# Kernel optimization log

Hardware: AMD Instinct MI355X
Metric: run time of the kernel (lower is better)

## Reference

```python
import jax, jax.numpy as jnp
import numpy as np
from jax import lax

KS = 3
PAD = 1


def setup_inputs() -> dict:
    key = jax.random.key(0)
    k1, k2, k3 = jax.random.split(key, 3)
    b, c, h, w = 8, 64, 128, 128
    out_c = 64
    x = jax.random.normal(k1, (b, c, h, w), dtype=jnp.float32)
    # small offset weights keep predicted offsets in a sane range
    w_off = jax.random.normal(k2, (2 * KS * KS, c, KS, KS), dtype=jnp.float32) * 0.05
    b_off = jnp.zeros((2 * KS * KS,), dtype=jnp.float32)
    w_reg = jax.random.normal(k3, (out_c, c * KS * KS), dtype=jnp.float32) * 0.02
    b_reg = jnp.zeros((out_c,), dtype=jnp.float32)
    return {"x": x, "w_off": w_off, "b_off": b_off, "w_reg": w_reg, "b_reg": b_reg}


def _deform_forward(x, w_off, b_off, w_reg, b_reg):
    ks, pad = KS, PAD
    b, c, h, w = x.shape
    # offset conv: 3x3, stride 1, pad 1 -> [b, 2*ks*ks, h, w]
    offset = lax.conv_general_dilated(
        x, w_off, window_strides=(1, 1), padding=[(pad, pad), (pad, pad)],
        dimension_numbers=("NCHW", "OIHW", "NCHW"))
    offset = offset + b_off[None, :, None, None]

    # pad input (zeros), as in the torch module
    xp = jnp.pad(x, ((0, 0), (0, 0), (pad, pad), (pad, pad)))
    Hp, Wp = h + 2 * pad, w + 2 * pad

    dt = x.dtype
    # base grid p0: [...,0] = column (x), [...,1] = row (y)
    yy, xx = jnp.meshgrid(jnp.arange(h, dtype=dt), jnp.arange(w, dtype=dt), indexing="ij")
    # kernel offsets p_n: flattened k = i*ks + j -> (lin[j], lin[i])
    lin = jnp.linspace(-(ks - 1) // 2, (ks - 1) // 2, ks).astype(dt)
    pn_i, pn_j = jnp.meshgrid(lin, lin, indexing="ij")
    pn = jnp.stack([pn_j, pn_i], axis=-1).reshape(ks * ks, 2)  # [ks2, 2]

    # offsets: [b, ks2, 2, h, w] -> [b, ks2, h, w, 2]; [...,0]=x off, [...,1]=y off
    off = offset.reshape(b, ks * ks, 2, h, w).transpose(0, 1, 3, 4, 2)

    px = xx[None, None] + pn[None, :, 0, None, None] + off[..., 0]  # [b, ks2, h, w]
    py = yy[None, None] + pn[None, :, 1, None, None] + off[..., 1]

    # torch normalizes by UNPADDED (w-1, h-1) but samples the PADDED tensor with
    # align_corners=True; reproduce exactly: q = p/(dim-1) * (dim_pad-1)
    qx = px / (w - 1) * (Wp - 1)
    qy = py / (h - 1) * (Hp - 1)

    x0 = jnp.floor(qx)
    y0 = jnp.floor(qy)
    wx1 = qx - x0  # frac weights
    wy1 = qy - y0
    wx0 = 1.0 - wx1
    wy0 = 1.0 - wy1
    ix0 = x0.astype(jnp.int32)
    iy0 = y0.astype(jnp.int32)
    ix1 = ix0 + 1
    iy1 = iy0 + 1

    def corner(iy, ix):
        valid = ((iy >= 0) & (iy < Hp) & (ix >= 0) & (ix < Wp)).astype(dt)
        iyc = jnp.clip(iy, 0, Hp - 1)
        ixc = jnp.clip(ix, 0, Wp - 1)
        # gather per batch: img [c,Hp,Wp], idx [ks2,h,w] -> [c,ks2,h,w]
        vals = jax.vmap(lambda img, a, bb: img[:, a, bb])(xp, iyc, ixc)
        return vals * valid[:, None]  # broadcast over channel dim

    v00 = corner(iy0, ix0)
    v01 = corner(iy0, ix1)
    v10 = corner(iy1, ix0)
    v11 = corner(iy1, ix1)

    wy0e = wy0[:, None]; wy1e = wy1[:, None]
    wx0e = wx0[:, None]; wx1e = wx1[:, None]
    sampled = (v00 * wy0e * wx0e + v01 * wy0e * wx1e +
               v10 * wy1e * wx0e + v11 * wy1e * wx1e)  # [b, c, ks2, h, w]

    # layout matches torch: [b, c*ks2, h, w] with (c, kk) order
    xs = sampled.reshape(b, c * ks * ks, h, w)
    out = jnp.einsum("bkhw,ok->bohw", xs, w_reg) + b_reg[None, :, None, None]
    return out


def reference(x, w_off, b_off, w_reg, b_reg):
    return _deform_forward(x, w_off, b_off, w_reg, b_reg)
```

## Files before the change

kernel.cpp:

```cpp
#include <hip/hip_runtime.h>
#include <math.h>

#define HH 128
#define WW 128
#define CC 64
#define BB 8
#define OC 64
#define OFFC 18
#define HW (HH*WW)
#define HP 136
#define WP 136
#define PHW (HP*WP)

typedef __attribute__((ext_vector_type(8))) _Float16 f16x8;
typedef __attribute__((ext_vector_type(4))) float f32x4;

#define P_OFF      0
#define P_SIZE     (BB*32*PHW)
#define OFFS_OFF   (P_OFF + P_SIZE)
#define OFFS_SIZE  (BB*OFFC*HW)
#define WAREG_OFF  (OFFS_OFF + OFFS_SIZE)
#define WAREG_SIZE 18432
#define WAOFF_OFF  (WAREG_OFF + WAREG_SIZE)

__device__ __forceinline__ unsigned short f2h(float f) {
    _Float16 t = (_Float16)f;
    unsigned short s;
    __builtin_memcpy(&s, &t, 2);
    return s;
}
__device__ __forceinline__ f16x8 u4_to_h8(uint4 u) {
    union { uint4 u; f16x8 h; } c; c.u = u; return c.h;
}
__device__ __forceinline__ uint4 h8_to_u4(f16x8 h) {
    union { uint4 u; f16x8 h; } c; c.h = h; return c.u;
}
__device__ __forceinline__ f16x8 splat8(float f) {
    _Float16 t = (_Float16)f;
    return (f16x8){t, t, t, t, t, t, t, t};
}

__global__ __launch_bounds__(256) void prep_kernel(
    const float* __restrict__ w_reg, const float* __restrict__ w_off,
    unsigned short* __restrict__ wA_reg, unsigned short* __restrict__ wA_off)
{
    int i = blockIdx.x * 256 + threadIdx.x;
    if (i < 18 * 64 * 32) {
        int j = i & 7, quad = (i >> 3) & 3, o = (i >> 5) & 63, ks = i >> 11;
        int kt = ks >> 1, kk = ks & 1;
        int c = kk * 32 + quad * 8 + j;
        wA_reg[i] = f2h(w_reg[o * 576 + c * 9 + kt]);
    }
    if (i < 18 * 32 * 32) {
        int j = i & 7, quad = (i >> 3) & 3, o = (i >> 5) & 31, ks = i >> 10;
        int kt = ks >> 1, kk = ks & 1;
        int c = kk * 32 + quad * 8 + j;
        float v = (o < OFFC) ? w_off[(o * CC + c) * 9 + kt] : 0.0f;
        wA_off[i] = f2h(v);
    }
}

__global__ __launch_bounds__(256) void pad_kernel(
    const float* __restrict__ x, uint4* __restrict__ P)
{
    int idx = blockIdx.x * 256 + threadIdx.x;
    if (idx >= BB * 8 * PHW) return;
    int pos = idx % PHW;
    int ig  = idx / PHW;
    int r   = pos / WP;
    int col = pos % WP;
    union { uint4 u; f16x8 h; } cv;
    cv.u = make_uint4(0u, 0u, 0u, 0u);
    if (r >= 4 && r <= 131 && col >= 4 && col <= 131) {
        const float* src = x + (ig * 8) * HW + (r - 4) * WW + (col - 4);
        #pragma unroll
        for (int e = 0; e < 8; ++e)
            cv.h[e] = (_Float16)src[e * HW];
    }
    P[idx] = cv.u;
}

__global__ __launch_bounds__(256) void offset_conv_kernel(
    const uint4* __restrict__ P, const unsigned short* __restrict__ wA_off,
    const float* __restrict__ b_off, float* __restrict__ offs)
{
    __shared__ uint4 xs[3 * 8 * 132];
    int img  = blockIdx.x & 7;
    int pblk = blockIdx.x >> 3;
    int tid  = threadIdx.x;
    const f16x8* wAv = (const f16x8*)wA_off;
    int lane = tid & 63;
    int wvid = tid >> 6;
    int s  = wvid & 1;
    int ph = wvid >> 1;

    for (int i = tid; i < 3 * 8 * 130; i += 256) {
        int r   = i / 1040;
        int rem = i - r * 1040;
        int g   = rem / 130;
        int j   = rem - g * 130;
        xs[(r * 8 + g) * 132 + j] =
            P[(img * 8 + g) * PHW + (pblk + 3 + r) * WP + (j + 3)];
    }
    __syncthreads();

    f32x4 acc[4];
    #pragma unroll
    for (int pt = 0; pt < 4; ++pt) acc[pt] = (f32x4){0.f, 0.f, 0.f, 0.f};

    const f16x8* xsv = (const f16x8*)xs;
    for (int tap = 0; tap < 9; ++tap) {
        int dy = tap / 3, dx = tap % 3;
        f16x8 a0 = wAv[((tap * 2 + 0) * 32 + s * 16 + (lane & 15)) * 4 + (lane >> 4)];
        f16x8 a1 = wAv[((tap * 2 + 1) * 32 + s * 16 + (lane & 15)) * 4 + (lane >> 4)];
        #pragma unroll
        for (int pt = 0; pt < 4; ++pt) {
            int j = ph * 64 + pt * 16 + (lane & 15) + dx;
            f16x8 b0 = xsv[(dy * 8 + (lane >> 4)) * 132 + j];
            acc[pt] = __builtin_amdgcn_mfma_f32_16x16x32_f16(a0, b0, acc[pt], 0, 0, 0);
            f16x8 b1 = xsv[(dy * 8 + 4 + (lane >> 4)) * 132 + j];
            acc[pt] = __builtin_amdgcn_mfma_f32_16x16x32_f16(a1, b1, acc[pt], 0, 0, 0);
        }
    }

    float* ob = offs + img * (OFFC * HW) + pblk * 128;
    #pragma unroll
    for (int r = 0; r < 4; ++r) {
        int o = s * 16 + (lane >> 4) * 4 + r;
        if (o < OFFC) {
            float bias = b_off[o];
            #pragma unroll
            for (int pt = 0; pt < 4; ++pt) {
                int pxl = ph * 64 + pt * 16 + (lane & 15);
                ob[o * HW + pxl] = acc[pt][r] + bias;
            }
        }
    }
}

__global__ __launch_bounds__(256) void deform_main_kernel(
    const uint4* __restrict__ P, const float* __restrict__ offs,
    const unsigned short* __restrict__ wA_reg, const float* __restrict__ b_reg,
    float* __restrict__ out)
{
    __shared__ uint4 xs2[2 * 512];
    int img  = blockIdx.x & 7;
    int rest = blockIdx.x >> 3;
    int half = rest & 1;
    int pblk = rest >> 1;
    int tid  = threadIdx.x;
    int pxl  = tid & 63;
    int qp   = tid >> 6;
    int wv = half * 64 + pxl;
    int hv = pblk;
    const float*  obf = offs + img * (OFFC * HW) + hv * WW + wv;
    const f16x8*  wAv = (const f16x8*)wA_reg;
    int lane = tid & 63;
    int wvid = tid >> 6;
    const float scale = 129.0f / 127.0f;

    f32x4 acc[4];
    #pragma unroll
    for (int pt = 0; pt < 4; ++pt) acc[pt] = (f32x4){0.f, 0.f, 0.f, 0.f};

    float offx = obf[0];
    float offy = obf[HW];

    for (int tap = 0; tap < 9; ++tap) {
        float offx_n = 0.f, offy_n = 0.f;
        if (tap < 8) {
            offx_n = obf[(2 * tap + 2) * HW];
            offy_n = obf[(2 * tap + 3) * HW];
        }
        f16x8 a0 = wAv[((tap * 2 + 0) * 64 + wvid * 16 + (lane & 15)) * 4 + (lane >> 4)];
        f16x8 a1 = wAv[((tap * 2 + 1) * 64 + wvid * 16 + (lane & 15)) * 4 + (lane >> 4)];

        float pxf = (float)wv + (float)(tap % 3 - 1) + offx;
        float pyf = (float)hv + (float)(tap / 3 - 1) + offy;
        float qx = fminf(fmaxf(pxf * scale, -100.0f), 300.0f);
        float qy = fminf(fmaxf(pyf * scale, -100.0f), 300.0f);
        float x0f = floorf(qx), y0f = floorf(qy);
        float wx1 = qx - x0f, wy1 = qy - y0f;
        float wx0 = 1.0f - wx1, wy0 = 1.0f - wy1;
        int ix0 = (int)x0f, iy0 = (int)y0f;
        int c0 = min(max(ix0 + 3, 0), WP - 2);
        int r0 = min(max(iy0 + 3, 0), HP - 1);
        int r1 = min(max(iy0 + 4, 0), HP - 1);
        int pr0 = r0 * WP + c0, pr1 = r1 * WP + c0;

        f16x8 wx0v = splat8(wx0), wx1v = splat8(wx1);
        f16x8 wy0v = splat8(wy0), wy1v = splat8(wy1);

        uint4* dst = xs2 + (tap & 1) * 512;
        #pragma unroll
        for (int gi = 0; gi < 2; ++gi) {
            int g = qp * 2 + gi;
            const uint4* xq = P + (img * 8 + g) * PHW;
            f16x8 v00 = u4_to_h8(xq[pr0]);
            f16x8 v01 = u4_to_h8(xq[pr0 + 1]);
            f16x8 v10 = u4_to_h8(xq[pr1]);
            f16x8 v11 = u4_to_h8(xq[pr1 + 1]);
            f16x8 row0 = v00 * wx0v + v01 * wx1v;
            f16x8 row1 = v10 * wx0v + v11 * wx1v;
            f16x8 sv   = row0 * wy0v + row1 * wy1v;
            dst[g * 64 + pxl] = h8_to_u4(sv);
        }
        __syncthreads();

        const f16x8* xsv = (const f16x8*)(xs2 + (tap & 1) * 512);
        #pragma unroll
        for (int pt = 0; pt < 4; ++pt) {
            int pxi = pt * 16 + (lane & 15);
            f16x8 b0 = xsv[(lane >> 4) * 64 + pxi];
            acc[pt] = __builtin_amdgcn_mfma_f32_16x16x32_f16(a0, b0, acc[pt], 0, 0, 0);
            f16x8 b1 = xsv[(4 + (lane >> 4)) * 64 + pxi];
            acc[pt] = __builtin_amdgcn_mfma_f32_16x16x32_f16(a1, b1, acc[pt], 0, 0, 0);
        }
        offx = offx_n;
        offy = offy_n;
    }

    float* op = out + img * (OC * HW) + hv * WW + half * 64;
    #pragma unroll
    for (int r = 0; r < 4; ++r) {
        int o = wvid * 16 + (lane >> 4) * 4 + r;
        float bias = b_reg[o];
        #pragma unroll
        for (int pt = 0; pt < 4; ++pt)
            op[o * HW + pt * 16 + (lane & 15)] = acc[pt][r] + bias;
    }
}

extern "C" void kernel_launch(void* const* d_in, const int* in_sizes, int n_in,
                              void* d_out, int out_size, void* d_ws, size_t ws_size,
                              hipStream_t stream) {
    const float* x     = (const float*)d_in[0];
    const float* w_off = (const float*)d_in[1];
    const float* b_off = (const float*)d_in[2];
    const float* w_reg = (const float*)d_in[3];
    const float* b_reg = (const float*)d_in[4];
    float* out = (float*)d_out;
    float* ws  = (float*)d_ws;

    uint4* P      = (uint4*)(ws + P_OFF);
    float* offs   = ws + OFFS_OFF;
    unsigned short* wA_reg = (unsigned short*)(ws + WAREG_OFF);
    unsigned short* wA_off = (unsigned short*)(ws + WAOFF_OFF);

    prep_kernel<<<144, 256, 0, stream>>>(w_reg, w_off, wA_reg, wA_off);
    pad_kernel<<<(BB * 8 * PHW + 255) / 256, 256, 0, stream>>>(x, P);
    offset_conv_kernel<<<1024, 256, 0, stream>>>(P, wA_off, b_off, offs);
    deform_main_kernel<<<2048, 256, 0, stream>>>(P, offs, wA_reg, b_reg, out);
}
```

Measured before the change: 156.6 us.

## Software-pipeline deformable gathers one tap ahead of the MFMA stage

Restructures the main deform kernel's tap loop so the bilinear-corner global loads for tap t+1, its weight fragments and the offsets two taps ahead are issued before the barrier and the MFMA work of tap t. The aim is to hide gather latency behind the matrix multiplies. The plain __syncthreads becomes an explicit lgkmcnt wait plus s_barrier so outstanding global loads are not drained at the barrier. It also unrolls the tap loop and adds a min-blocks hint of 4 to launch_bounds. The cost is more registers for the in-flight gather data, which may cause spills or reduce occupancy.

```diff
diff --git a/kernel.cpp b/kernel.cpp
--- a/kernel.cpp
+++ b/kernel.cpp
@@ -138,7 +138,52 @@
     }
 }
 
-__global__ __launch_bounds__(256) void deform_main_kernel(
+
+struct Gather8 {
+    uint4 a00, a01, a10, a11;
+    uint4 b00, b01, b10, b11;
+    float wx1, wy1;
+};
+
+__device__ __forceinline__ Gather8 issue_tap(
+    const uint4* __restrict__ xq0, const uint4* __restrict__ xq1,
+    int wv, int hv, int dx, int dy, float offx, float offy)
+{
+    const float scale = 129.0f / 127.0f;
+    float pxf = ((float)wv + (float)dx) + offx;
+    float pyf = ((float)hv + (float)dy) + offy;
+    float qx = fminf(fmaxf(pxf * scale, -100.0f), 300.0f);
+    float qy = fminf(fmaxf(pyf * scale, -100.0f), 300.0f);
+    float x0f = floorf(qx), y0f = floorf(qy);
+    Gather8 g;
+    g.wx1 = qx - x0f;
+    g.wy1 = qy - y0f;
+    int ix0 = (int)x0f, iy0 = (int)y0f;
+    int c0 = min(max(ix0 + 3, 0), WP - 2);
+    int r0 = min(max(iy0 + 3, 0), HP - 1);
+    int r1 = min(max(iy0 + 4, 0), HP - 1);
+    int pr0 = r0 * WP + c0, pr1 = r1 * WP + c0;
+    g.a00 = xq0[pr0]; g.a01 = xq0[pr0 + 1];
+    g.a10 = xq0[pr1]; g.a11 = xq0[pr1 + 1];
+    g.b00 = xq1[pr0]; g.b01 = xq1[pr0 + 1];
+    g.b10 = xq1[pr1]; g.b11 = xq1[pr1 + 1];
+    return g;
+}
+
+__device__ __forceinline__ void blend_write(
+    uint4* __restrict__ dst, int qp, int pxl, const Gather8& g)
+{
+    f16x8 wx1v = splat8(g.wx1), wx0v = splat8(1.0f - g.wx1);
+    f16x8 wy1v = splat8(g.wy1), wy0v = splat8(1.0f - g.wy1);
+    f16x8 r0a = u4_to_h8(g.a00) * wx0v + u4_to_h8(g.a01) * wx1v;
+    f16x8 r1a = u4_to_h8(g.a10) * wx0v + u4_to_h8(g.a11) * wx1v;
+    dst[(qp * 2 + 0) * 64 + pxl] = h8_to_u4(r0a * wy0v + r1a * wy1v);
+    f16x8 r0b = u4_to_h8(g.b00) * wx0v + u4_to_h8(g.b01) * wx1v;
+    f16x8 r1b = u4_to_h8(g.b10) * wx0v + u4_to_h8(g.b11) * wx1v;
+    dst[(qp * 2 + 1) * 64 + pxl] = h8_to_u4(r0b * wy0v + r1b * wy1v);
+}
+
+__global__ __launch_bounds__(256, 4) void deform_main_kernel(
     const uint4* __restrict__ P, const float* __restrict__ offs,
     const unsigned short* __restrict__ wA_reg, const float* __restrict__ b_reg,
     float* __restrict__ out)
@@ -157,67 +202,58 @@
     const f16x8*  wAv = (const f16x8*)wA_reg;
     int lane = tid & 63;
     int wvid = tid >> 6;
-    const float scale = 129.0f / 127.0f;
+    const uint4* xq0 = P + (img * 8 + qp * 2 + 0) * PHW;
+    const uint4* xq1 = P + (img * 8 + qp * 2 + 1) * PHW;
+    int aidx = (wvid * 16 + (lane & 15)) * 4 + (lane >> 4);
 
     f32x4 acc[4];
     #pragma unroll
     for (int pt = 0; pt < 4; ++pt) acc[pt] = (f32x4){0.f, 0.f, 0.f, 0.f};
 
-    float offx = obf[0];
-    float offy = obf[HW];
-
+    float ox0 = obf[0],      oy0 = obf[HW];
+    float ox1 = obf[2 * HW], oy1 = obf[3 * HW];
+    Gather8 cur = issue_tap(xq0, xq1, wv, hv, -1, -1, ox0, oy0);
+    f16x8 a0c = wAv[0 * 64 * 4 + aidx];
+    f16x8 a1c = wAv[1 * 64 * 4 + aidx];
+
+    #pragma unroll
     for (int tap = 0; tap < 9; ++tap) {
-        float offx_n = 0.f, offy_n = 0.f;
+        uint4* dst = xs2 + (tap & 1) * 512;
+        blend_write(dst, qp, pxl, cur);
+
+        float ox2 = 0.f, oy2 = 0.f;
+        if (tap < 7) {
+            ox2 = obf[(2 * tap + 4) * HW];
+            oy2 = obf[(2 * tap + 5) * HW];
+        }
+
+        Gather8 nxt;
+        f16x8 a0n, a1n;
         if (tap < 8) {
-            offx_n = obf[(2 * tap + 2) * HW];
-            offy_n = obf[(2 * tap + 3) * HW];
-        }
-        f16x8 a0 = wAv[((tap * 2 + 0) * 64 + wvid * 16 + (lane & 15)) * 4 + (lane >> 4)];
-        f16x8 a1 = wAv[((tap * 2 + 1) * 64 + wvid * 16 + (lane & 15)) * 4 + (lane >> 4)];
-
-        float pxf = (float)wv + (float)(tap % 3 - 1) + offx;
-        float pyf = (float)hv + (float)(tap / 3 - 1) + offy;
-        float qx = fminf(fmaxf(pxf * scale, -100.0f), 300.0f);
-        float qy = fminf(fmaxf(pyf * scale, -100.0f), 300.0f);
-        float x0f = floorf(qx), y0f = floorf(qy);
-        float wx1 = qx - x0f, wy1 = qy - y0f;
-        float wx0 = 1.0f - wx1, wy0 = 1.0f - wy1;
-        int ix0 = (int)x0f, iy0 = (int)y0f;
-        int c0 = min(max(ix0 + 3, 0), WP - 2);
-        int r0 = min(max(iy0 + 3, 0), HP - 1);
-        int r1 = min(max(iy0 + 4, 0), HP - 1);
-        int pr0 = r0 * WP + c0, pr1 = r1 * WP + c0;
-
-        f16x8 wx0v = splat8(wx0), wx1v = splat8(wx1);
-        f16x8 wy0v = splat8(wy0), wy1v = splat8(wy1);
-
-        uint4* dst = xs2 + (tap & 1) * 512;
-        #pragma unroll
-        for (int gi = 0; gi < 2; ++gi) {
-            int g = qp * 2 + gi;
-            const uint4* xq = P + (img * 8 + g) * PHW;
-            f16x8 v00 = u4_to_h8(xq[pr0]);
-            f16x8 v01 = u4_to_h8(xq[pr0 + 1]);
-            f16x8 v10 = u4_to_h8(xq[pr1]);
-            f16x8 v11 = u4_to_h8(xq[pr1 + 1]);
-            f16x8 row0 = v00 * wx0v + v01 * wx1v;
-            f16x8 row1 = v10 * wx0v + v11 * wx1v;
-            f16x8 sv   = row0 * wy0v + row1 * wy1v;
-            dst[g * 64 + pxl] = h8_to_u4(sv);
-        }
-        __syncthreads();
+            int dx1 = (tap + 1) % 3 - 1, dy1 = (tap + 1) / 3 - 1;
+            nxt = issue_tap(xq0, xq1, wv, hv, dx1, dy1, ox1, oy1);
+            a0n = wAv[((tap + 1) * 2 + 0) * 64 * 4 + aidx];
+            a1n = wAv[((tap + 1) * 2 + 1) * 64 * 4 + aidx];
+        }
+
+        asm volatile("s_waitcnt lgkmcnt(0)" ::: "memory");
+        __builtin_amdgcn_s_barrier();
+        asm volatile("" ::: "memory");
 
         const f16x8* xsv = (const f16x8*)(xs2 + (tap & 1) * 512);
         #pragma unroll
         for (int pt = 0; pt < 4; ++pt) {
             int pxi = pt * 16 + (lane & 15);
             f16x8 b0 = xsv[(lane >> 4) * 64 + pxi];
-            acc[pt] = __builtin_amdgcn_mfma_f32_16x16x32_f16(a0, b0, acc[pt], 0, 0, 0);
+            acc[pt] = __builtin_amdgcn_mfma_f32_16x16x32_f16(a0c, b0, acc[pt], 0, 0, 0);
             f16x8 b1 = xsv[(4 + (lane >> 4)) * 64 + pxi];
-            acc[pt] = __builtin_amdgcn_mfma_f32_16x16x32_f16(a1, b1, acc[pt], 0, 0, 0);
-        }
-        offx = offx_n;
-        offy = offy_n;
+            acc[pt] = __builtin_amdgcn_mfma_f32_16x16x32_f16(a1c, b1, acc[pt], 0, 0, 0);
+        }
+
+        if (tap < 8) {
+            cur = nxt; a0c = a0n; a1c = a1n;
+            ox1 = ox2; oy1 = oy2;
+        }
     }
 
     float* op = out + img * (OC * HW) + hv * WW + half * 64;
```

Result: no change. 155.1 us (-1.0%).
